# Kernel optimization log

Measured on AMD Instinct MI355X. Metric: run time of the kernel, lower is better.

Reference implementation:

```python
import jax, jax.numpy as jnp
import numpy as np

N_NODES = 100000
N_EDGES = 3200000
N_GRAPHS = 2048
VOCAB = 92
H = 64
N_LAYERS = 3


def setup_inputs() -> dict:
    key = jax.random.key(0)
    ks = jax.random.split(key, 16)
    x = jax.random.randint(ks[0], (N_NODES,), 0, VOCAB)
    edge_index = jax.random.randint(ks[1], (2, N_EDGES), 0, N_NODES)
    batch = jnp.sort(jax.random.randint(ks[2], (N_NODES,), 0, N_GRAPHS))
    s = 0.1
    return {
        "x": x,
        "edge_index": edge_index,
        "batch": batch,
        "emb": jax.random.normal(ks[3], (VOCAB, H), jnp.float32) * s,
        "conv_w": jax.random.normal(ks[4], (N_LAYERS, H, H), jnp.float32) * s,
        "conv_b": jax.random.normal(ks[5], (N_LAYERS, H), jnp.float32) * s,
        "w1": jax.random.normal(ks[6], (H, H // 2), jnp.float32) * s,
        "b1": jax.random.normal(ks[7], (H // 2,), jnp.float32) * s,
        "w2": jax.random.normal(ks[8], (H // 2, H // 4), jnp.float32) * s,
        "b2": jax.random.normal(ks[9], (H // 4,), jnp.float32) * s,
        "w3": jax.random.normal(ks[10], (H // 4, 1), jnp.float32) * s,
        "b3": jax.random.normal(ks[11], (1,), jnp.float32) * s,
    }


def _gcn_graph(edge_index, n_nodes):
    # add self-loops, then symmetric degree normalization (PyG GCNConv default)
    loop = jnp.arange(n_nodes)
    row = jnp.concatenate([edge_index[0], loop])  # source
    col = jnp.concatenate([edge_index[1], loop])  # target (aggregation index)
    deg = jnp.zeros((n_nodes,), jnp.float32).at[col].add(1.0)
    dinv = jnp.where(deg > 0, jax.lax.rsqrt(deg), 0.0)
    norm = dinv[row] * dinv[col]  # [E+N]
    return row, col, norm


def _forward(x, edge_index, batch, emb, conv_w, conv_b, w1, b1, w2, b2, w3, b3):
    n = x.shape[0]
    row, col, norm = _gcn_graph(edge_index, n)
    h = emb[x]  # [N,H] embedding lookup
    for i in range(N_LAYERS):
        t = h @ conv_w[i]  # linear transform first (GCNConv)
        msg = t[row] * norm[:, None]  # gather + edge scaling
        agg = jax.ops.segment_sum(msg, col, num_segments=n)  # scatter-add
        h_new = jax.nn.relu(agg + conv_b[i])
        h = h_new if i == 0 else h + h_new  # residual after first layer
    # global mean pool over graphs
    sums = jax.ops.segment_sum(h, batch, num_segments=N_GRAPHS)
    cnt = jax.ops.segment_sum(jnp.ones((n,), h.dtype), batch, num_segments=N_GRAPHS)
    g = sums / jnp.maximum(cnt, 1.0)[:, None]  # [G,H]
    # predictor MLP (dropout is identity in eval)
    g = jax.nn.relu(g @ w1 + b1)
    g = jax.nn.relu(g @ w2 + b2)
    return g @ w3 + b3  # [G,1]


def reference(x, edge_index, batch, emb, conv_w, conv_b, w1, b1, w2, b2, w3, b3):
    return _forward(x, edge_index, batch, emb, conv_w, conv_b, w1, b1, w2, b2, w3, b3)
```

## Files before the change

### kernel.cpp

```cpp
#include <hip/hip_runtime.h>

#define N_NODES 100000
#define N_EDGES 3200000
#define N_GRAPHS 2048
#define VOCAB 92
#define H 64
#define N_LAYERS 3

#define BUCK_BITS 7
#define BUCK_NODES (1 << BUCK_BITS)
#define NBUCK ((N_NODES + BUCK_NODES - 1) / BUCK_NODES)

#define PART_BLOCKS 256
#define EDGES_PER_PART (N_EDGES / PART_BLOCKS)

#define G0_TILE 64
#define SBINS_STRIDE 100
#define SB_STRIDE 104

#define FL_TILE 64
#define A_STRIDE 72

typedef _Float16 half8 __attribute__((ext_vector_type(8)));
typedef float f32x4 __attribute__((ext_vector_type(4)));

__device__ inline unsigned short f2bf(float f) {
    union { float f; unsigned u; } v; v.f = f;
    unsigned u = v.u;
    u += 0x7fffu + ((u >> 16) & 1u);
    return (unsigned short)(u >> 16);
}
__device__ inline float bfhi(unsigned p) {
    union { unsigned u; float f; } v; v.u = p & 0xffff0000u; return v.f;
}
__device__ inline float bflo(unsigned p) {
    union { unsigned u; float f; } v; v.u = p << 16; return v.f;
}

__device__ inline void unpack_add(uint4 v, float* a) {
    a[0] += bflo(v.x); a[1] += bfhi(v.x);
    a[2] += bflo(v.y); a[3] += bfhi(v.y);
    a[4] += bflo(v.z); a[5] += bfhi(v.z);
    a[6] += bflo(v.w); a[7] += bfhi(v.w);
}


__global__ void k_init(int* bcnt, int* srpad) {
    int i = threadIdx.x;
    if (i < NBUCK) bcnt[i] = 0;
    if (i < 16) srpad[i] = 0;
}

__global__ void k_bhist(const int* __restrict__ col, int* __restrict__ bcnt,
                        int* __restrict__ blkhist) {
    __shared__ int lh[NBUCK];
    int tid = threadIdx.x;
    for (int i = tid; i < NBUCK; i += 256) lh[i] = 0;
    __syncthreads();
    int base = blockIdx.x * EDGES_PER_PART;
    for (int k = tid; k < EDGES_PER_PART; k += 256)
        atomicAdd(&lh[col[base + k] >> BUCK_BITS], 1);
    __syncthreads();
    int* myhist = blkhist + (size_t)blockIdx.x * NBUCK;
    for (int i = tid; i < NBUCK; i += 256) {
        int c = lh[i];
        myhist[i] = c;
        if (c) atomicAdd(&bcnt[i], c);
    }
}

__global__ void k_bscan(const int* __restrict__ bcnt, int* __restrict__ bbase,
                        int* __restrict__ bcur) {
    __shared__ int s[1024];
    int tid = threadIdx.x;
    int v = (tid < NBUCK) ? bcnt[tid] : 0;
    s[tid] = v;
    __syncthreads();
    for (int off = 1; off < 1024; off <<= 1) {
        int x = (tid >= off) ? s[tid - off] : 0;
        __syncthreads();
        s[tid] += x;
        __syncthreads();
    }
    if (tid < NBUCK) {
        int e = s[tid] - v;
        bbase[tid] = e;
        bcur[tid] = e;
    }
    if (tid == 0) bbase[NBUCK] = N_EDGES;
}

__global__ __launch_bounds__(1024) void k_binA(const int* __restrict__ row,
                                               const int* __restrict__ col,
                                               const int* __restrict__ blkhist,
                                               int* __restrict__ bcur,
                                               int* __restrict__ staging) {
    __shared__ int lcnt[NBUCK];
    __shared__ int lbase[NBUCK];
    int tid = threadIdx.x;
    int base = blockIdx.x * EDGES_PER_PART;
    const int* myhist = blkhist + (size_t)blockIdx.x * NBUCK;
    for (int i = tid; i < NBUCK; i += 1024) {
        int c = myhist[i];
        lbase[i] = c ? atomicAdd(&bcur[i], c) : 0;
        lcnt[i] = 0;
    }
    __syncthreads();
    for (int k = tid; k < EDGES_PER_PART; k += 1024) {
        int c = col[base + k];
        int b = c >> BUCK_BITS;
        int r = atomicAdd(&lcnt[b], 1);
        staging[lbase[b] + r] = row[base + k] | ((c & (BUCK_NODES - 1)) << 17);
    }
}

__global__ void k_binB(const int* __restrict__ staging, const int* __restrict__ bbase,
                       const int* __restrict__ x,
                       int* __restrict__ sorted_row, int* __restrict__ degi,
                       int* __restrict__ row_start, float* __restrict__ dinv,
                       unsigned* __restrict__ packed) {
    __shared__ int lde[BUCK_NODES];
    __shared__ int lsc[BUCK_NODES];
    int b = blockIdx.x, tid = threadIdx.x;
    int n0 = b << BUCK_BITS;
    int s0 = bbase[b], s1 = bbase[b + 1];
    if (tid < BUCK_NODES) lde[tid] = 0;
    __syncthreads();
    for (int i = s0 + tid; i < s1; i += 256)
        atomicAdd(&lde[staging[i] >> 17], 1);
    __syncthreads();
    if (tid < BUCK_NODES) lsc[tid] = lde[tid];
    __syncthreads();
    for (int off = 1; off < BUCK_NODES; off <<= 1) {
        int v = (tid >= off && tid < BUCK_NODES) ? lsc[tid - off] : 0;
        __syncthreads();
        if (tid < BUCK_NODES) lsc[tid] += v;
        __syncthreads();
    }
    if (tid < BUCK_NODES) {
        int n = n0 + tid;
        int excl = lsc[tid] - lde[tid];
        if (n < N_NODES) {
            row_start[n] = s0 + excl;
            degi[n] = lde[tid];
            float dv = rsqrtf((float)(lde[tid] + 1));
            dinv[n] = dv;
            packed[n] = ((unsigned)f2bf(dv) << 16) | (unsigned)x[n];
        }
        lsc[tid] = excl;
        lde[tid] = 0;
    }
    __syncthreads();
    for (int i = s0 + tid; i < s1; i += 256) {
        int p = staging[i];
        int ln = p >> 17;
        int r = atomicAdd(&lde[ln], 1);
        sorted_row[s0 + lsc[ln] + r] = p & 0x1FFFF;
    }
}

__global__ void k_premix(const float* __restrict__ emb, const float* __restrict__ W0,
                         float* __restrict__ M) {
    int v = blockIdx.x, c = threadIdx.x;
    float acc = 0.0f;
#pragma unroll
    for (int k = 0; k < H; ++k) acc += emb[v * H + k] * W0[k * H + c];
    M[v * H + c] = acc;
}

__global__ __launch_bounds__(256) void k_gather0_mfma(
    const int* __restrict__ sorted_row, const int* __restrict__ row_start,
    const int* __restrict__ degi, const unsigned* __restrict__ packed,
    const float* __restrict__ M, const float* __restrict__ dinv,
    const float* __restrict__ bias, float* __restrict__ h,
    unsigned short* __restrict__ qout) {
    __shared__ float Sbins[G0_TILE][SBINS_STRIDE];
    __shared__ _Float16 Sb[G0_TILE][SB_STRIDE];
    __shared__ _Float16 Blds[H][SB_STRIDE];
    __shared__ int sstart[G0_TILE];
    __shared__ int sdeg[G0_TILE];

    int tid = threadIdx.x;
    int n0 = blockIdx.x * G0_TILE;

    for (int i = tid; i < G0_TILE * SBINS_STRIDE; i += 256)
        ((float*)Sbins)[i] = 0.0f;
    {
        int c = tid & 63, v0 = tid >> 6;
        for (int v = v0; v < VOCAB; v += 4)
            Blds[c][v] = (_Float16)M[v * H + c];
        Blds[c][VOCAB + v0] = (_Float16)0.0f;
    }
    if (tid < G0_TILE) {
        int n = n0 + tid;
        sdeg[tid] = (n < N_NODES) ? degi[n] : 0;
        sstart[tid] = (n < N_NODES) ? row_start[n] : 0;
    }
    __syncthreads();

    int w = tid >> 6, lane = tid & 63;

    if (tid < G0_TILE) {
        int n = n0 + tid;
        if (n < N_NODES) {
            unsigned p = packed[n];
            atomicAdd(&Sbins[tid][p & 127u], __uint_as_float(p & 0xffff0000u));
        }
    }
    for (int ni = 0; ni < 16; ++ni) {
        int nl = (w << 4) + ni;
        int d = sdeg[nl];
        int st = sstart[nl];
        for (int e = lane; e < d; e += 64) {
            unsigned p = packed[sorted_row[st + e]];
            atomicAdd(&Sbins[nl][p & 127u], __uint_as_float(p & 0xffff0000u));
        }
    }
    __syncthreads();

    {
        int r0 = tid >> 2, k0 = (tid & 3) * 24;
#pragma unroll
        for (int m = 0; m < 3; ++m) {
            f32x4 f0 = *(const f32x4*)&Sbins[r0][k0 + 8 * m];
            f32x4 f1 = *(const f32x4*)&Sbins[r0][k0 + 8 * m + 4];
            half8 o;
            o[0] = (_Float16)f0[0]; o[1] = (_Float16)f0[1];
            o[2] = (_Float16)f0[2]; o[3] = (_Float16)f0[3];
            o[4] = (_Float16)f1[0]; o[5] = (_Float16)f1[1];
            o[6] = (_Float16)f1[2]; o[7] = (_Float16)f1[3];
            *(half8*)&Sb[r0][k0 + 8 * m] = o;
        }
    }
    __syncthreads();

    int l15 = lane & 15, l4 = lane >> 4;
    half8 afr[3];
#pragma unroll
    for (int ks = 0; ks < 3; ++ks)
        afr[ks] = *(const half8*)&Sb[(w << 4) + l15][ks * 32 + l4 * 8];

    f32x4 acc[4];
#pragma unroll
    for (int c = 0; c < 4; ++c) {
        f32x4 a = {0.0f, 0.0f, 0.0f, 0.0f};
#pragma unroll
        for (int ks = 0; ks < 3; ++ks) {
            half8 bfr = *(const half8*)&Blds[c * 16 + l15][ks * 32 + l4 * 8];
            a = __builtin_amdgcn_mfma_f32_16x16x32_f16(afr[ks], bfr, a, 0, 0, 0);
        }
        acc[c] = a;
    }

    int rbase = (w << 4) + l4 * 4;
    float di4[4];
#pragma unroll
    for (int r = 0; r < 4; ++r) {
        int n = n0 + rbase + r;
        di4[r] = (n < N_NODES) ? dinv[n] : 0.0f;
    }
#pragma unroll
    for (int c = 0; c < 4; ++c) {
        float bb = bias[c * 16 + l15];
#pragma unroll
        for (int r = 0; r < 4; ++r) {
            int n = n0 + rbase + r;
            if (n < N_NODES) {
                float v = fmaxf(acc[c][r] * di4[r] + bb, 0.0f);
                h[(size_t)n * H + c * 16 + l15] = v;
                qout[(size_t)n * H + c * 16 + l15] = f2bf(di4[r] * v);
            }
        }
    }
}

__global__ __launch_bounds__(512) void k_fused(
    const int* __restrict__ sorted_row, const int* __restrict__ row_start,
    const int* __restrict__ degi, const unsigned* __restrict__ q,
    const float* __restrict__ dinv, const float* __restrict__ W,
    const float* __restrict__ bias, float* __restrict__ h,
    unsigned short* __restrict__ qout, int last) {
    __shared__ _Float16 Alds[FL_TILE][A_STRIDE];
    __shared__ _Float16 Blds[H][A_STRIDE];

    int tid = threadIdx.x;
    int n0 = blockIdx.x * FL_TILE;

    {
        int c = tid & 63, k0 = (tid >> 6) * 8;
#pragma unroll
        for (int k = 0; k < 8; ++k)
            Blds[c][k0 + k] = (_Float16)W[(k0 + k) * H + c];
    }

    int w = tid >> 6, lane = tid & 63;
    int s = lane >> 3;
    int j = lane & 7;
    const uint4* q4 = (const uint4*)q;

    for (int ni = 0; ni < 8; ++ni) {
        int nl = (w << 3) + ni;
        int n = n0 + nl;
        int d = 0, st = 0;
        if (n < N_NODES) { d = degi[n]; st = row_start[n]; }
        const int* srp = sorted_row + st;
        float a[8];
#pragma unroll
        for (int k = 0; k < 8; ++k) a[k] = 0.0f;

        int srA = srp[s];
        int srB = srp[8 + s];
        int e = 0;
        for (; e + 16 <= d; e += 16) {
            uint4 va = q4[(size_t)srA * 8 + j];
            uint4 vb = q4[(size_t)srB * 8 + j];
            srA = srp[e + 16 + s];
            srB = srp[e + 24 + s];
            unpack_add(va, a);
            unpack_add(vb, a);
        }
        if (e < d) {
            uint4 va = q4[(size_t)srA * 8 + j];
            uint4 vb = q4[(size_t)srB * 8 + j];
            if (e + s >= d) { va.x = 0; va.y = 0; va.z = 0; va.w = 0; }
            if (e + 8 + s >= d) { vb.x = 0; vb.y = 0; vb.z = 0; vb.w = 0; }
            unpack_add(va, a);
            unpack_add(vb, a);
        }
#pragma unroll
        for (int k = 0; k < 8; ++k) a[k] += __shfl_xor(a[k], 8, 64);
#pragma unroll
        for (int k = 0; k < 8; ++k) a[k] += __shfl_xor(a[k], 16, 64);
#pragma unroll
        for (int k = 0; k < 8; ++k) a[k] += __shfl_xor(a[k], 32, 64);
        if (s == 0) {
            if (n < N_NODES) {
                uint4 vs = q4[(size_t)n * 8 + j];
                unpack_add(vs, a);
            }
            half8 o;
#pragma unroll
            for (int k = 0; k < 8; ++k) o[k] = (_Float16)a[k];
            *(half8*)&Alds[nl][j * 8] = o;
        }
    }
    __syncthreads();

    int l15 = lane & 15, l4 = lane >> 4;
    int rw = (w & 3) << 4;
    int cb = (w >> 2) << 1;
    half8 afr[2];
#pragma unroll
    for (int ks = 0; ks < 2; ++ks)
        afr[ks] = *(const half8*)&Alds[rw + l15][ks * 32 + l4 * 8];

    f32x4 acc[2];
#pragma unroll
    for (int ci = 0; ci < 2; ++ci) {
        f32x4 a = {0.0f, 0.0f, 0.0f, 0.0f};
#pragma unroll
        for (int ks = 0; ks < 2; ++ks) {
            half8 bfr = *(const half8*)&Blds[(cb + ci) * 16 + l15][ks * 32 + l4 * 8];
            a = __builtin_amdgcn_mfma_f32_16x16x32_f16(afr[ks], bfr, a, 0, 0, 0);
        }
        acc[ci] = a;
    }

    int rbase = rw + l4 * 4;
    float di4[4];
#pragma unroll
    for (int r = 0; r < 4; ++r) {
        int n = n0 + rbase + r;
        di4[r] = (n < N_NODES) ? dinv[n] : 0.0f;
    }
#pragma unroll
    for (int ci = 0; ci < 2; ++ci) {
        float bb = bias[(cb + ci) * 16 + l15];
#pragma unroll
        for (int r = 0; r < 4; ++r) {
            int n = n0 + rbase + r;
            if (n < N_NODES) {
                size_t idx = (size_t)n * H + (cb + ci) * 16 + l15;
                float v = h[idx] + fmaxf(acc[ci][r] * di4[r] + bb, 0.0f);
                h[idx] = v;
                if (!last) qout[idx] = f2bf(di4[r] * v);
            }
        }
    }
}

__global__ void k_poolmlp(const float* __restrict__ h, const int* __restrict__ batch,
                          const float* __restrict__ w1, const float* __restrict__ b1,
                          const float* __restrict__ w2, const float* __restrict__ b2,
                          const float* __restrict__ w3, const float* __restrict__ b3,
                          float* __restrict__ out) {
    __shared__ float sg[H];
    __shared__ float s1[32];
    __shared__ float s2[16];
    int g = blockIdx.x, tid = threadIdx.x;
    int lo = 0, hi = N_NODES;
    while (lo < hi) { int mid = (lo + hi) >> 1; if (batch[mid] < g) lo = mid + 1; else hi = mid; }
    int lo2 = lo, hi2 = N_NODES;
    while (lo2 < hi2) { int mid = (lo2 + hi2) >> 1; if (batch[mid] < g + 1) lo2 = mid + 1; else hi2 = mid; }
    float acc = 0.0f;
    for (int n = lo; n < lo2; ++n) acc += h[(size_t)n * H + tid];
    float cntf = (float)(lo2 - lo);
    sg[tid] = acc / fmaxf(cntf, 1.0f);
    __syncthreads();
    if (tid < 32) {
        float a = b1[tid];
#pragma unroll
        for (int k = 0; k < H; ++k) a += sg[k] * w1[k * 32 + tid];
        s1[tid] = fmaxf(a, 0.0f);
    }
    __syncthreads();
    if (tid < 16) {
        float a = b2[tid];
#pragma unroll
        for (int k = 0; k < 32; ++k) a += s1[k] * w2[k * 16 + tid];
        s2[tid] = fmaxf(a, 0.0f);
    }
    __syncthreads();
    if (tid == 0) {
        float a = b3[0];
#pragma unroll
        for (int k = 0; k < 16; ++k) a += s2[k] * w3[k];
        out[g] = a;
    }
}


extern "C" void kernel_launch(void* const* d_in, const int* in_sizes, int n_in,
                              void* d_out, int out_size, void* d_ws, size_t ws_size,
                              hipStream_t stream) {
    const int*   x      = (const int*)d_in[0];
    const int*   eidx   = (const int*)d_in[1];
    const int*   batch  = (const int*)d_in[2];
    const float* emb    = (const float*)d_in[3];
    const float* conv_w = (const float*)d_in[4];
    const float* conv_b = (const float*)d_in[5];
    const float* w1     = (const float*)d_in[6];
    const float* b1     = (const float*)d_in[7];
    const float* w2     = (const float*)d_in[8];
    const float* b2     = (const float*)d_in[9];
    const float* w3     = (const float*)d_in[10];
    const float* b3     = (const float*)d_in[11];
    float* out = (float*)d_out;

    const int* row = eidx;
    const int* col = eidx + N_EDGES;

    char* wsb = (char*)d_ws;
    size_t off = 0;
    auto alloc = [&](size_t elems) { void* p = wsb + off; off += ((elems * 4 + 255) & ~(size_t)255); return p; };
    int*      bcnt       = (int*)alloc(NBUCK);
    int*      bbase      = (int*)alloc(NBUCK + 1);
    int*      bcur       = (int*)alloc(NBUCK);
    int*      blkhist    = (int*)alloc((size_t)PART_BLOCKS * NBUCK);
    int*      row_start  = (int*)alloc(N_NODES);
    int*      degi       = (int*)alloc(N_NODES);
    float*    dinv       = (float*)alloc(N_NODES);
    unsigned* packed     = (unsigned*)alloc(N_NODES);
    float*    M          = (float*)alloc(VOCAB * H);
    int*      sorted_row = (int*)alloc(N_EDGES + 16);
    float*    h          = (float*)alloc((size_t)N_NODES * H);
    unsigned short* qa   = (unsigned short*)alloc((size_t)N_NODES * H / 2);
    unsigned short* qb   = (unsigned short*)alloc((size_t)N_NODES * H / 2);

    int* staging = (int*)qa;

    const int B = 256;
    const int gT = (N_NODES + G0_TILE - 1) / G0_TILE;
    const int gF = (N_NODES + FL_TILE - 1) / FL_TILE;

    hipLaunchKernelGGL(k_init, dim3(1), dim3(1024), 0, stream, bcnt, sorted_row + N_EDGES);
    hipLaunchKernelGGL(k_bhist, dim3(PART_BLOCKS), dim3(256), 0, stream, col, bcnt, blkhist);
    hipLaunchKernelGGL(k_bscan, dim3(1), dim3(1024), 0, stream, bcnt, bbase, bcur);
    hipLaunchKernelGGL(k_binA, dim3(PART_BLOCKS), dim3(1024), 0, stream,
                       row, col, blkhist, bcur, staging);
    hipLaunchKernelGGL(k_binB, dim3(NBUCK), dim3(256), 0, stream, staging, bbase, x,
                       sorted_row, degi, row_start, dinv, packed);

    hipLaunchKernelGGL(k_premix, dim3(VOCAB), dim3(H), 0, stream, emb, conv_w, M);
    hipLaunchKernelGGL(k_gather0_mfma, dim3(gT), dim3(B), 0, stream,
                       sorted_row, row_start, degi, packed, M, dinv, conv_b, h, qa);

    hipLaunchKernelGGL(k_fused, dim3(gF), dim3(512), 0, stream,
                       sorted_row, row_start, degi, (const unsigned*)qa, dinv,
                       conv_w + (size_t)1 * H * H, conv_b + 1 * H, h, qb, 0);
    hipLaunchKernelGGL(k_fused, dim3(gF), dim3(512), 0, stream,
                       sorted_row, row_start, degi, (const unsigned*)qb, dinv,
                       conv_w + (size_t)2 * H * H, conv_b + 2 * H, h, qa, 1);

    hipLaunchKernelGGL(k_poolmlp, dim3(N_GRAPHS), dim3(64), 0, stream,
                       h, batch, w1, b1, w2, b2, w3, b3, out);

    (void)in_sizes; (void)n_in; (void)out_size; (void)ws_size;
}
```

Measured before the change: 380.8 us.

## Store residual hidden state in bf16 and drop separate init/atomic bucket count

The residual hidden state h is now stored as bf16 instead of fp32, which halves its read/write traffic in the fused layers and the pooling kernel. Separately, the k_init kernel and the global atomic bucket counting are removed. The scan kernel now sums the per-block histograms itself and zeroes the sorted_row padding. The cost is that residual accumulation is rounded to bf16, and the single-block scan does a serial 256-step loop per bucket.

```diff
diff --git a/kernel.cpp b/kernel.cpp
--- a/kernel.cpp
+++ b/kernel.cpp
@@ -36,6 +36,9 @@
 __device__ inline float bflo(unsigned p) {
     union { unsigned u; float f; } v; v.u = p << 16; return v.f;
 }
+__device__ inline float bf2f(unsigned short b) {
+    union { unsigned u; float f; } v; v.u = ((unsigned)b) << 16; return v.f;
+}
 
 __device__ inline void unpack_add(uint4 v, float* a) {
     a[0] += bflo(v.x); a[1] += bfhi(v.x);
@@ -45,14 +48,7 @@
 }
 
 
-__global__ void k_init(int* bcnt, int* srpad) {
-    int i = threadIdx.x;
-    if (i < NBUCK) bcnt[i] = 0;
-    if (i < 16) srpad[i] = 0;
-}
-
-__global__ void k_bhist(const int* __restrict__ col, int* __restrict__ bcnt,
-                        int* __restrict__ blkhist) {
+__global__ void k_bhist(const int* __restrict__ col, int* __restrict__ blkhist) {
     __shared__ int lh[NBUCK];
     int tid = threadIdx.x;
     for (int i = tid; i < NBUCK; i += 256) lh[i] = 0;
@@ -62,18 +58,18 @@
         atomicAdd(&lh[col[base + k] >> BUCK_BITS], 1);
     __syncthreads();
     int* myhist = blkhist + (size_t)blockIdx.x * NBUCK;
-    for (int i = tid; i < NBUCK; i += 256) {
-        int c = lh[i];
-        myhist[i] = c;
-        if (c) atomicAdd(&bcnt[i], c);
-    }
-}
-
-__global__ void k_bscan(const int* __restrict__ bcnt, int* __restrict__ bbase,
-                        int* __restrict__ bcur) {
+    for (int i = tid; i < NBUCK; i += 256) myhist[i] = lh[i];
+}
+
+__global__ void k_bscan(const int* __restrict__ blkhist, int* __restrict__ bbase,
+                        int* __restrict__ bcur, int* __restrict__ srpad) {
     __shared__ int s[1024];
     int tid = threadIdx.x;
-    int v = (tid < NBUCK) ? bcnt[tid] : 0;
+    if (tid < 64) srpad[tid] = 0;
+    int v = 0;
+    if (tid < NBUCK) {
+        for (int b = 0; b < PART_BLOCKS; ++b) v += blkhist[(size_t)b * NBUCK + tid];
+    }
     s[tid] = v;
     __syncthreads();
     for (int off = 1; off < 1024; off <<= 1) {
@@ -172,7 +168,7 @@
     const int* __restrict__ sorted_row, const int* __restrict__ row_start,
     const int* __restrict__ degi, const unsigned* __restrict__ packed,
     const float* __restrict__ M, const float* __restrict__ dinv,
-    const float* __restrict__ bias, float* __restrict__ h,
+    const float* __restrict__ bias, unsigned short* __restrict__ h,
     unsigned short* __restrict__ qout) {
     __shared__ float Sbins[G0_TILE][SBINS_STRIDE];
     __shared__ _Float16 Sb[G0_TILE][SB_STRIDE];
@@ -267,7 +263,7 @@
             int n = n0 + rbase + r;
             if (n < N_NODES) {
                 float v = fmaxf(acc[c][r] * di4[r] + bb, 0.0f);
-                h[(size_t)n * H + c * 16 + l15] = v;
+                h[(size_t)n * H + c * 16 + l15] = f2bf(v);
                 qout[(size_t)n * H + c * 16 + l15] = f2bf(di4[r] * v);
             }
         }
@@ -278,7 +274,7 @@
     const int* __restrict__ sorted_row, const int* __restrict__ row_start,
     const int* __restrict__ degi, const unsigned* __restrict__ q,
     const float* __restrict__ dinv, const float* __restrict__ W,
-    const float* __restrict__ bias, float* __restrict__ h,
+    const float* __restrict__ bias, unsigned short* __restrict__ h,
     unsigned short* __restrict__ qout, int last) {
     __shared__ _Float16 Alds[FL_TILE][A_STRIDE];
     __shared__ _Float16 Blds[H][A_STRIDE];
@@ -381,15 +377,16 @@
             int n = n0 + rbase + r;
             if (n < N_NODES) {
                 size_t idx = (size_t)n * H + (cb + ci) * 16 + l15;
-                float v = h[idx] + fmaxf(acc[ci][r] * di4[r] + bb, 0.0f);
-                h[idx] = v;
+                float v = bf2f(h[idx]) + fmaxf(acc[ci][r] * di4[r] + bb, 0.0f);
+                h[idx] = f2bf(v);
                 if (!last) qout[idx] = f2bf(di4[r] * v);
             }
         }
     }
 }
 
-__global__ void k_poolmlp(const float* __restrict__ h, const int* __restrict__ batch,
+__global__ void k_poolmlp(const unsigned short* __restrict__ h,
+                          const int* __restrict__ batch,
                           const float* __restrict__ w1, const float* __restrict__ b1,
                           const float* __restrict__ w2, const float* __restrict__ b2,
                           const float* __restrict__ w3, const float* __restrict__ b3,
@@ -403,7 +400,7 @@
     int lo2 = lo, hi2 = N_NODES;
     while (lo2 < hi2) { int mid = (lo2 + hi2) >> 1; if (batch[mid] < g + 1) lo2 = mid + 1; else hi2 = mid; }
     float acc = 0.0f;
-    for (int n = lo; n < lo2; ++n) acc += h[(size_t)n * H + tid];
+    for (int n = lo; n < lo2; ++n) acc += bf2f(h[(size_t)n * H + tid]);
     float cntf = (float)(lo2 - lo);
     sg[tid] = acc / fmaxf(cntf, 1.0f);
     __syncthreads();
@@ -453,7 +450,6 @@
     char* wsb = (char*)d_ws;
     size_t off = 0;
     auto alloc = [&](size_t elems) { void* p = wsb + off; off += ((elems * 4 + 255) & ~(size_t)255); return p; };
-    int*      bcnt       = (int*)alloc(NBUCK);
     int*      bbase      = (int*)alloc(NBUCK + 1);
     int*      bcur       = (int*)alloc(NBUCK);
     int*      blkhist    = (int*)alloc((size_t)PART_BLOCKS * NBUCK);
@@ -462,8 +458,8 @@
     float*    dinv       = (float*)alloc(N_NODES);
     unsigned* packed     = (unsigned*)alloc(N_NODES);
     float*    M          = (float*)alloc(VOCAB * H);
-    int*      sorted_row = (int*)alloc(N_EDGES + 16);
-    float*    h          = (float*)alloc((size_t)N_NODES * H);
+    int*      sorted_row = (int*)alloc(N_EDGES + 64);
+    unsigned short* h    = (unsigned short*)alloc((size_t)N_NODES * H / 2);
     unsigned short* qa   = (unsigned short*)alloc((size_t)N_NODES * H / 2);
     unsigned short* qb   = (unsigned short*)alloc((size_t)N_NODES * H / 2);
 
@@ -473,9 +469,9 @@
     const int gT = (N_NODES + G0_TILE - 1) / G0_TILE;
     const int gF = (N_NODES + FL_TILE - 1) / FL_TILE;
 
-    hipLaunchKernelGGL(k_init, dim3(1), dim3(1024), 0, stream, bcnt, sorted_row + N_EDGES);
-    hipLaunchKernelGGL(k_bhist, dim3(PART_BLOCKS), dim3(256), 0, stream, col, bcnt, blkhist);
-    hipLaunchKernelGGL(k_bscan, dim3(1), dim3(1024), 0, stream, bcnt, bbase, bcur);
+    hipLaunchKernelGGL(k_bhist, dim3(PART_BLOCKS), dim3(256), 0, stream, col, blkhist);
+    hipLaunchKernelGGL(k_bscan, dim3(1), dim3(1024), 0, stream,
+                       blkhist, bbase, bcur, sorted_row + N_EDGES);
     hipLaunchKernelGGL(k_binA, dim3(PART_BLOCKS), dim3(1024), 0, stream,
                        row, col, blkhist, bcur, staging);
     hipLaunchKernelGGL(k_binB, dim3(NBUCK), dim3(256), 0, stream, staging, bbase, x,
```

Measured after the change: 379.0 us. No clear change (-0.5%).

## Shrink buckets to 64 nodes, gather layer 0 from staging, store h in bf16

Applied to the files above, without the earlier changes.

Halves the bucket size so each layer-0 block maps to one bucket. Layer 0 now reads the bucketed staging array directly, with contiguous edge iteration and less per-node degree imbalance, instead of walking per-node sorted lists. The residual state h is stored in bf16 instead of fp32, which halves its read/write traffic in the fused layers and the pool. Buffers are swapped so staging (aliased to qa) is not overwritten before layer 0 consumes it. The risks are lower accuracy in the residual accumulation and more buckets, hence more histogram and scan work.

```diff
diff --git a/kernel.cpp b/kernel.cpp
--- a/kernel.cpp
+++ b/kernel.cpp
@@ -7,7 +7,7 @@
 #define H 64
 #define N_LAYERS 3
 
-#define BUCK_BITS 7
+#define BUCK_BITS 6
 #define BUCK_NODES (1 << BUCK_BITS)
 #define NBUCK ((N_NODES + BUCK_NODES - 1) / BUCK_NODES)
 
@@ -36,6 +36,9 @@
 __device__ inline float bflo(unsigned p) {
     union { unsigned u; float f; } v; v.u = p << 16; return v.f;
 }
+__device__ inline float bf2f(unsigned short b) {
+    union { unsigned u; float f; } v; v.u = ((unsigned)b) << 16; return v.f;
+}
 
 __device__ inline void unpack_add(uint4 v, float* a) {
     a[0] += bflo(v.x); a[1] += bfhi(v.x);
@@ -47,8 +50,8 @@
 
 __global__ void k_init(int* bcnt, int* srpad) {
     int i = threadIdx.x;
-    if (i < NBUCK) bcnt[i] = 0;
-    if (i < 16) srpad[i] = 0;
+    for (int k = i; k < NBUCK; k += 1024) bcnt[k] = 0;
+    if (i < 64) srpad[i] = 0;
 }
 
 __global__ void k_bhist(const int* __restrict__ col, int* __restrict__ bcnt,
@@ -71,22 +74,22 @@
 
 __global__ void k_bscan(const int* __restrict__ bcnt, int* __restrict__ bbase,
                         int* __restrict__ bcur) {
-    __shared__ int s[1024];
+    __shared__ int s[2048];
     int tid = threadIdx.x;
-    int v = (tid < NBUCK) ? bcnt[tid] : 0;
-    s[tid] = v;
-    __syncthreads();
-    for (int off = 1; off < 1024; off <<= 1) {
-        int x = (tid >= off) ? s[tid - off] : 0;
+    int p0 = tid, p1 = tid + 1024;
+    int v0 = (p0 < NBUCK) ? bcnt[p0] : 0;
+    int v1 = (p1 < NBUCK) ? bcnt[p1] : 0;
+    s[p0] = v0; s[p1] = v1;
+    __syncthreads();
+    for (int off = 1; off < 2048; off <<= 1) {
+        int t0 = (p0 >= off) ? s[p0 - off] : 0;
+        int t1 = (p1 >= off) ? s[p1 - off] : 0;
         __syncthreads();
-        s[tid] += x;
+        s[p0] += t0; s[p1] += t1;
         __syncthreads();
     }
-    if (tid < NBUCK) {
-        int e = s[tid] - v;
-        bbase[tid] = e;
-        bcur[tid] = e;
-    }
+    if (p0 < NBUCK) { int e = s[p0] - v0; bbase[p0] = e; bcur[p0] = e; }
+    if (p1 < NBUCK) { int e = s[p1] - v1; bbase[p1] = e; bcur[p1] = e; }
     if (tid == 0) bbase[NBUCK] = N_EDGES;
 }
 
@@ -169,19 +172,18 @@
 }
 
 __global__ __launch_bounds__(256) void k_gather0_mfma(
-    const int* __restrict__ sorted_row, const int* __restrict__ row_start,
-    const int* __restrict__ degi, const unsigned* __restrict__ packed,
+    const int* __restrict__ staging, const int* __restrict__ bbase,
+    const unsigned* __restrict__ packed,
     const float* __restrict__ M, const float* __restrict__ dinv,
-    const float* __restrict__ bias, float* __restrict__ h,
+    const float* __restrict__ bias, unsigned short* __restrict__ h,
     unsigned short* __restrict__ qout) {
     __shared__ float Sbins[G0_TILE][SBINS_STRIDE];
     __shared__ _Float16 Sb[G0_TILE][SB_STRIDE];
     __shared__ _Float16 Blds[H][SB_STRIDE];
-    __shared__ int sstart[G0_TILE];
-    __shared__ int sdeg[G0_TILE];
 
     int tid = threadIdx.x;
-    int n0 = blockIdx.x * G0_TILE;
+    int b = blockIdx.x;
+    int n0 = b << BUCK_BITS;
 
     for (int i = tid; i < G0_TILE * SBINS_STRIDE; i += 256)
         ((float*)Sbins)[i] = 0.0f;
@@ -191,14 +193,7 @@
             Blds[c][v] = (_Float16)M[v * H + c];
         Blds[c][VOCAB + v0] = (_Float16)0.0f;
     }
-    if (tid < G0_TILE) {
-        int n = n0 + tid;
-        sdeg[tid] = (n < N_NODES) ? degi[n] : 0;
-        sstart[tid] = (n < N_NODES) ? row_start[n] : 0;
-    }
-    __syncthreads();
-
-    int w = tid >> 6, lane = tid & 63;
+    __syncthreads();
 
     if (tid < G0_TILE) {
         int n = n0 + tid;
@@ -207,13 +202,21 @@
             atomicAdd(&Sbins[tid][p & 127u], __uint_as_float(p & 0xffff0000u));
         }
     }
-    for (int ni = 0; ni < 16; ++ni) {
-        int nl = (w << 4) + ni;
-        int d = sdeg[nl];
-        int st = sstart[nl];
-        for (int e = lane; e < d; e += 64) {
-            unsigned p = packed[sorted_row[st + e]];
-            atomicAdd(&Sbins[nl][p & 127u], __uint_as_float(p & 0xffff0000u));
+    {
+        int s0 = bbase[b], s1 = bbase[b + 1];
+        int i = s0 + tid;
+        for (; i + 256 < s1; i += 512) {
+            int p0 = staging[i];
+            int p1 = staging[i + 256];
+            unsigned k0 = packed[p0 & 0x1FFFF];
+            unsigned k1 = packed[p1 & 0x1FFFF];
+            atomicAdd(&Sbins[p0 >> 17][k0 & 127u], __uint_as_float(k0 & 0xffff0000u));
+            atomicAdd(&Sbins[p1 >> 17][k1 & 127u], __uint_as_float(k1 & 0xffff0000u));
+        }
+        if (i < s1) {
+            int p0 = staging[i];
+            unsigned k0 = packed[p0 & 0x1FFFF];
+            atomicAdd(&Sbins[p0 >> 17][k0 & 127u], __uint_as_float(k0 & 0xffff0000u));
         }
     }
     __syncthreads();
@@ -234,6 +237,7 @@
     }
     __syncthreads();
 
+    int w = tid >> 6, lane = tid & 63;
     int l15 = lane & 15, l4 = lane >> 4;
     half8 afr[3];
 #pragma unroll
@@ -267,7 +271,7 @@
             int n = n0 + rbase + r;
             if (n < N_NODES) {
                 float v = fmaxf(acc[c][r] * di4[r] + bb, 0.0f);
-                h[(size_t)n * H + c * 16 + l15] = v;
+                h[(size_t)n * H + c * 16 + l15] = f2bf(v);
                 qout[(size_t)n * H + c * 16 + l15] = f2bf(di4[r] * v);
             }
         }
@@ -278,7 +282,7 @@
     const int* __restrict__ sorted_row, const int* __restrict__ row_start,
     const int* __restrict__ degi, const unsigned* __restrict__ q,
     const float* __restrict__ dinv, const float* __restrict__ W,
-    const float* __restrict__ bias, float* __restrict__ h,
+    const float* __restrict__ bias, unsigned short* __restrict__ h,
     unsigned short* __restrict__ qout, int last) {
     __shared__ _Float16 Alds[FL_TILE][A_STRIDE];
     __shared__ _Float16 Blds[H][A_STRIDE];
@@ -381,15 +385,16 @@
             int n = n0 + rbase + r;
             if (n < N_NODES) {
                 size_t idx = (size_t)n * H + (cb + ci) * 16 + l15;
-                float v = h[idx] + fmaxf(acc[ci][r] * di4[r] + bb, 0.0f);
-                h[idx] = v;
+                float v = bf2f(h[idx]) + fmaxf(acc[ci][r] * di4[r] + bb, 0.0f);
+                h[idx] = f2bf(v);
                 if (!last) qout[idx] = f2bf(di4[r] * v);
             }
         }
     }
 }
 
-__global__ void k_poolmlp(const float* __restrict__ h, const int* __restrict__ batch,
+__global__ void k_poolmlp(const unsigned short* __restrict__ h,
+                          const int* __restrict__ batch,
                           const float* __restrict__ w1, const float* __restrict__ b1,
                           const float* __restrict__ w2, const float* __restrict__ b2,
                           const float* __restrict__ w3, const float* __restrict__ b3,
@@ -403,7 +408,7 @@
     int lo2 = lo, hi2 = N_NODES;
     while (lo2 < hi2) { int mid = (lo2 + hi2) >> 1; if (batch[mid] < g + 1) lo2 = mid + 1; else hi2 = mid; }
     float acc = 0.0f;
-    for (int n = lo; n < lo2; ++n) acc += h[(size_t)n * H + tid];
+    for (int n = lo; n < lo2; ++n) acc += bf2f(h[(size_t)n * H + tid]);
     float cntf = (float)(lo2 - lo);
     sg[tid] = acc / fmaxf(cntf, 1.0f);
     __syncthreads();
@@ -462,15 +467,14 @@
     float*    dinv       = (float*)alloc(N_NODES);
     unsigned* packed     = (unsigned*)alloc(N_NODES);
     float*    M          = (float*)alloc(VOCAB * H);
-    int*      sorted_row = (int*)alloc(N_EDGES + 16);
-    float*    h          = (float*)alloc((size_t)N_NODES * H);
+    int*      sorted_row = (int*)alloc(N_EDGES + 64);
+    unsigned short* h    = (unsigned short*)alloc((size_t)N_NODES * H / 2);
     unsigned short* qa   = (unsigned short*)alloc((size_t)N_NODES * H / 2);
     unsigned short* qb   = (unsigned short*)alloc((size_t)N_NODES * H / 2);
 
     int* staging = (int*)qa;
 
     const int B = 256;
-    const int gT = (N_NODES + G0_TILE - 1) / G0_TILE;
     const int gF = (N_NODES + FL_TILE - 1) / FL_TILE;
 
     hipLaunchKernelGGL(k_init, dim3(1), dim3(1024), 0, stream, bcnt, sorted_row + N_EDGES);
@@ -482,15 +486,15 @@
                        sorted_row, degi, row_start, dinv, packed);
 
     hipLaunchKernelGGL(k_premix, dim3(VOCAB), dim3(H), 0, stream, emb, conv_w, M);
-    hipLaunchKernelGGL(k_gather0_mfma, dim3(gT), dim3(B), 0, stream,
-                       sorted_row, row_start, degi, packed, M, dinv, conv_b, h, qa);
-
+    hipLaunchKernelGGL(k_gather0_mfma, dim3(NBUCK), dim3(B), 0, stream,
+                       staging, bbase, packed, M, dinv, conv_b, h, qb);
+
+    hipLaunchKernelGGL(k_fused, dim3(gF), dim3(512), 0, stream,
+                       sorted_row, row_start, degi, (const unsigned*)qb, dinv,
+                       conv_w + (size_t)1 * H * H, conv_b + 1 * H, h, qa, 0);
     hipLaunchKernelGGL(k_fused, dim3(gF), dim3(512), 0, stream,
                        sorted_row, row_start, degi, (const unsigned*)qa, dinv,
-                       conv_w + (size_t)1 * H * H, conv_b + 1 * H, h, qb, 0);
-    hipLaunchKernelGGL(k_fused, dim3(gF), dim3(512), 0, stream,
-                       sorted_row, row_start, degi, (const unsigned*)qb, dinv,
-                       conv_w + (size_t)2 * H * H, conv_b + 2 * H, h, qa, 1);
+                       conv_w + (size_t)2 * H * H, conv_b + 2 * H, h, qb, 1);
 
     hipLaunchKernelGGL(k_poolmlp, dim3(N_GRAPHS), dim3(64), 0, stream,
                        h, batch, w1, b1, w2, b2, w3, b3, out);
```

New measurement: 363.3 us. 4.6% less time.
